# Performance work log

Measured on AMD Instinct MI355X. Metric: run time of the kernel, lower is better.

## Reference

```python
import jax, jax.numpy as jnp
import numpy as np

ROLE_BITS = 20
NHEAD = 16
D_MODEL = 1024
D_KEY = D_MODEL // NHEAD  # 64
D_FIL = 512
DFF = 4096
EPS = 1e-5


def _ln(x, g, b):
    mu = jnp.mean(x, axis=-1, keepdims=True)
    var = jnp.mean(jnp.square(x - mu), axis=-1, keepdims=True)
    return (x - mu) * jax.lax.rsqrt(var + EPS) * g + b


def setup_inputs() -> dict:
    key = jax.random.key(0)
    ks = jax.random.split(key, 10)
    N, BSZ, MEM = 16384, 16, 8
    D_IN = D_FIL + ROLE_BITS  # 532
    values = jax.random.normal(ks[0], (N, D_FIL), jnp.float32)
    role_index = jax.random.randint(ks[1], (N,), 1, 2 ** ROLE_BITS)
    # every (batch, memory_slot) pair occupied -> static shapes (compression is a no-op)
    slot = jax.random.permutation(ks[2], jnp.tile(jnp.arange(BSZ * MEM), N // (BSZ * MEM)))
    batch_index = (slot // MEM).astype(jnp.int32)
    memory_index = (slot % MEM).astype(jnp.int32)
    query_vectors = jax.random.normal(ks[3], (NHEAD, D_KEY), jnp.float32) * (1.0 / np.sqrt(D_KEY))
    s = 0.02
    Wk = jax.random.normal(ks[4], (D_MODEL, D_IN), jnp.float32) * s
    Wv = jax.random.normal(ks[5], (D_MODEL, D_IN), jnp.float32) * s
    Wo = jax.random.normal(ks[6], (D_MODEL, D_MODEL), jnp.float32) * s
    W1 = jax.random.normal(ks[7], (DFF, D_MODEL), jnp.float32) * s
    W2 = jax.random.normal(ks[8], (D_MODEL, DFF), jnp.float32) * s
    return dict(
        values=values, role_index=role_index, batch_index=batch_index,
        memory_index=memory_index, query_vectors=query_vectors,
        Wk=Wk, Wv=Wv, Wo=Wo, bo=jnp.zeros((D_MODEL,), jnp.float32),
        W1=W1, b1=jnp.zeros((DFF,), jnp.float32),
        W2=W2, b2=jnp.zeros((D_MODEL,), jnp.float32),
        g_fil=jnp.ones((D_FIL,), jnp.float32), b_fil=jnp.zeros((D_FIL,), jnp.float32),
        g_mha=jnp.ones((D_IN,), jnp.float32), b_mha=jnp.zeros((D_IN,), jnp.float32),
        g_ff=jnp.ones((D_MODEL,), jnp.float32), b_ff=jnp.zeros((D_MODEL,), jnp.float32),
        g_out=jnp.ones((D_MODEL,), jnp.float32), b_out=jnp.zeros((D_MODEL,), jnp.float32),
        bsz=BSZ, memory_slots=MEM,
    )


def _tree_positional_encodings(role_index):
    # bit-expand role indices: column j is bit j of the role index
    bits = (jnp.bitwise_and(role_index[:, None], 2 ** jnp.arange(ROLE_BITS)) != 0).astype(jnp.float32)
    # locate the highest set bit (torch: flip + argmax)
    mi = jnp.argmax(bits[:, ::-1], axis=1)
    cm = ROLE_BITS - 1 - mi  # index of highest set bit
    bits = bits * (1.0 - jax.nn.one_hot(cm, ROLE_BITS, dtype=bits.dtype))  # zero it out
    branch = jnp.arange(ROLE_BITS)[None, :] < cm[:, None]
    return jnp.where(branch, (bits - 0.5) * 2.0, bits)  # {0,1} -> {-1,1} below MSB


def reference(values, role_index, batch_index, memory_index, query_vectors,
              Wk, Wv, Wo, bo, W1, b1, W2, b2,
              g_fil, b_fil, g_mha, b_mha, g_ff, b_ff, g_out, b_out,
              bsz, memory_slots):
    N = values.shape[0]
    T = bsz * memory_slots  # num_trees (all (batch, slot) pairs occupied)

    tpd = _tree_positional_encodings(role_index)
    x = jnp.concatenate([_ln(values, g_fil, b_fil), tpd], axis=1)  # [N, d_input]
    x = _ln(x, g_mha, b_mha)
    k = (x @ Wk.T).reshape(N, NHEAD, D_KEY)
    v = (x @ Wv.T).reshape(N, NHEAD, D_KEY)
    qkm = jnp.einsum('nhd,hd->nh', k, query_vectors)  # [N, H]

    # combined batch+memory mask: node n attends to flat tree t = b*mem + m
    node_slot = batch_index * memory_slots + memory_index  # [N]
    mask = node_slot[:, None] == jnp.arange(T)[None, :]  # [N, T]
    scores = jnp.where(mask[:, :, None], qkm[:, None, :], -1e9) / np.sqrt(D_KEY)
    attn = jax.nn.softmax(scores, axis=0)  # softmax over nodes, [N, T, H]
    out = jnp.einsum('nhv,nth->thv', v, attn).reshape(T, D_MODEL)

    # post-attention: proj_o + residual with flattened queries, LN, FF, LN
    r1 = (out @ Wo.T + bo) + query_vectors.reshape(-1)
    l1 = _ln(r1, g_ff, b_ff)
    ff = jax.nn.gelu(l1 @ W1.T + b1, approximate=False) @ W2.T + b2
    l2 = _ln(ff + r1, g_out, b_out)

    rectangle_out = l2.reshape(bsz, memory_slots, D_MODEL)
    agent_pad_mask = jnp.zeros((bsz, memory_slots), dtype=bool)
    return rectangle_out, agent_pad_mask
```

## Files before the change

### kernel.cpp

```cpp
#include <hip/hip_runtime.h>
#include <hip/hip_bf16.h>

typedef __hip_bfloat16 bf16;

#define N_NODES 16384
#define D_FIL 512
#define D_IN 532
#define D_MODEL 1024
#define NHEAD 16
#define D_KEY 64
#define DFF 4096
#define NTREE 128
#define MEM_SLOTS 8
#define NODES_PER_TREE 128
#define EPS 1e-5f
#define XSE 544
#define XSU 272
#define CSTR 32
#define BSTR 40

typedef float f32x4 __attribute__((ext_vector_type(4)));
typedef short s16x8 __attribute__((ext_vector_type(8)));

union PackU { uint4 u; s16x8 s; };

__device__ inline float gelu_exact(float x) {
    return 0.5f * x * (1.0f + erff(x * 0.7071067811865476f));
}

__device__ inline void blockReduceSum2(float& a, float& b, float* sm) {
    int tid = threadIdx.x;
    int lane = tid & 63, wid = tid >> 6;
#pragma unroll
    for (int off = 32; off > 0; off >>= 1) {
        a += __shfl_down(a, off, 64);
        b += __shfl_down(b, off, 64);
    }
    if (lane == 0) { sm[wid] = a; sm[4 + wid] = b; }
    __syncthreads();
    if (tid == 0) {
        sm[8] = sm[0] + sm[1] + sm[2] + sm[3];
        sm[9] = sm[4] + sm[5] + sm[6] + sm[7];
    }
    __syncthreads();
    a = sm[8]; b = sm[9];
}

__global__ __launch_bounds__(256) void prep_kernel(
        const float* __restrict__ values, const int* __restrict__ role,
        const int* __restrict__ bidx, const int* __restrict__ midx,
        const float* __restrict__ g_fil, const float* __restrict__ b_fil,
        const float* __restrict__ g_mha, const float* __restrict__ b_mha,
        bf16* __restrict__ xs, int* __restrict__ counts,
        const float* __restrict__ q, const float* __restrict__ Wk,
        unsigned* __restrict__ wqb,
        const float* __restrict__ Wv, float* __restrict__ wvt) {
    int b = blockIdx.x;
    int tid = threadIdx.x;

    if (b < 16) {
        int h = b;
        __shared__ float qs[64];
        if (tid < 64) qs[tid] = q[h * 64 + tid];
        __syncthreads();
        for (int p = tid; p < XSU; p += 256) {
            unsigned out = 0u;
            if (p < 266) {
                float a0 = 0.f, a1 = 0.f;
                int j0 = 2 * p;
#pragma unroll 8
                for (int d = 0; d < 64; ++d) {
                    const float* wr = Wk + (size_t)(h * 64 + d) * D_IN;
                    a0 += qs[d] * wr[j0];
                    a1 += qs[d] * wr[j0 + 1];
                }
                unsigned u0 = (unsigned)__bfloat16_as_ushort(__float2bfloat16(a0));
                unsigned u1 = (unsigned)__bfloat16_as_ushort(__float2bfloat16(a1));
                out = (u1 << 16) | u0;
            }
            wqb[h * XSU + p] = out;
        }
        return;
    }

    if (b < 560) {
        __shared__ float tile[32][33];
        int vb = b - 16;
        int c0 = (vb & 31) * 32, j0 = (vb >> 5) * 32;
        int tx = tid & 31, ty = tid >> 5;
#pragma unroll
        for (int r = 0; r < 4; ++r) {
            int cc = ty + r * 8;
            int j = j0 + tx;
            tile[cc][tx] = (j < D_IN) ? Wv[(size_t)(c0 + cc) * D_IN + j] : 0.f;
        }
        __syncthreads();
#pragma unroll
        for (int r = 0; r < 4; ++r) {
            int j = j0 + ty + r * 8;
            if (j < D_IN) wvt[(size_t)j * D_MODEL + c0 + tx] = tile[tx][ty + r * 8];
        }
        return;
    }

    int wave = tid >> 6;
    int l = tid & 63;
    int n = (b - 560) * 4 + wave;

    const float4* vp = (const float4*)(values + (size_t)n * D_FIL + l * 8);
    float4 v0 = vp[0], v1 = vp[1];

    int row = 0;
    if (l == 0) {
        int slot = bidx[n] * MEM_SLOTS + midx[n];
        int pos = atomicAdd(&counts[slot * CSTR], 1);
        row = slot * NODES_PER_TREE + pos;
    }

    float s = v0.x + v0.y + v0.z + v0.w + v1.x + v1.y + v1.z + v1.w;
    float ss = v0.x * v0.x + v0.y * v0.y + v0.z * v0.z + v0.w * v0.w
             + v1.x * v1.x + v1.y * v1.y + v1.z * v1.z + v1.w * v1.w;
#pragma unroll
    for (int m = 1; m < 64; m <<= 1) {
        s += __shfl_xor(s, m, 64);
        ss += __shfl_xor(ss, m, 64);
    }
    float mu = s * (1.f / D_FIL);
    float var = ss * (1.f / D_FIL) - mu * mu;
    float rs = rsqrtf(var + EPS);

    const float4* gf = (const float4*)(g_fil + l * 8);
    const float4* bf = (const float4*)(b_fil + l * 8);
    float4 gf0 = gf[0], gf1 = gf[1], bf0 = bf[0], bf1 = bf[1];
    float y[8];
    y[0] = (v0.x - mu) * rs * gf0.x + bf0.x;
    y[1] = (v0.y - mu) * rs * gf0.y + bf0.y;
    y[2] = (v0.z - mu) * rs * gf0.z + bf0.z;
    y[3] = (v0.w - mu) * rs * gf0.w + bf0.w;
    y[4] = (v1.x - mu) * rs * gf1.x + bf1.x;
    y[5] = (v1.y - mu) * rs * gf1.y + bf1.y;
    y[6] = (v1.z - mu) * rs * gf1.z + bf1.z;
    y[7] = (v1.w - mu) * rs * gf1.w + bf1.w;

    int r = role[n];
    int cm = 31 - __clz(r);
    float s_t = 2.f * (float)(__popc(r) - 1) - (float)cm;
    float ss_t = (float)cm;

    float s2 = y[0] + y[1] + y[2] + y[3] + y[4] + y[5] + y[6] + y[7];
    float ss2 = y[0] * y[0] + y[1] * y[1] + y[2] * y[2] + y[3] * y[3]
              + y[4] * y[4] + y[5] * y[5] + y[6] * y[6] + y[7] * y[7];
#pragma unroll
    for (int m = 1; m < 64; m <<= 1) {
        s2 += __shfl_xor(s2, m, 64);
        ss2 += __shfl_xor(ss2, m, 64);
    }
    s2 += s_t; ss2 += ss_t;
    float mu2 = s2 * (1.f / D_IN);
    float var2 = ss2 * (1.f / D_IN) - mu2 * mu2;
    float rs2 = rsqrtf(var2 + EPS);

    const float4* gm = (const float4*)(g_mha + l * 8);
    const float4* bm = (const float4*)(b_mha + l * 8);
    float4 gm0 = gm[0], gm1 = gm[1], bm0 = bm[0], bm1 = bm[1];
    float x[8];
    x[0] = (y[0] - mu2) * rs2 * gm0.x + bm0.x;
    x[1] = (y[1] - mu2) * rs2 * gm0.y + bm0.y;
    x[2] = (y[2] - mu2) * rs2 * gm0.z + bm0.z;
    x[3] = (y[3] - mu2) * rs2 * gm0.w + bm0.w;
    x[4] = (y[4] - mu2) * rs2 * gm1.x + bm1.x;
    x[5] = (y[5] - mu2) * rs2 * gm1.y + bm1.y;
    x[6] = (y[6] - mu2) * rs2 * gm1.z + bm1.z;
    x[7] = (y[7] - mu2) * rs2 * gm1.w + bm1.w;

    row = __shfl(row, 0, 64);

    {
        unsigned us[8];
#pragma unroll
        for (int k = 0; k < 8; ++k)
            us[k] = (unsigned)__bfloat16_as_ushort(__float2bfloat16(x[k]));
        uint4 pk = make_uint4((us[1] << 16) | us[0], (us[3] << 16) | us[2],
                              (us[5] << 16) | us[4], (us[7] << 16) | us[6]);
        *(uint4*)((char*)xs + (size_t)row * (XSE * 2) + 16 * l) = pk;
    }

    if (l < 20) {
        int bit = (r >> l) & 1;
        float tpd = (l < cm) ? (bit ? 1.f : -1.f) : 0.f;
        float x2 = (tpd - mu2) * rs2 * g_mha[512 + l] + b_mha[512 + l];
        xs[(size_t)row * XSE + 512 + l] = __float2bfloat16(x2);
    } else if (l < 26) {
        ((unsigned*)xs)[(size_t)row * XSU + 266 + (l - 20)] = 0u;
    }
}

__global__ __launch_bounds__(256) void qkm_kernel(const unsigned* __restrict__ xsu,
                                                  const unsigned* __restrict__ wqb,
                                                  float* __restrict__ qkmp) {
    __shared__ unsigned wshw[16 * 274];
    int tid = threadIdx.x;
#pragma unroll
    for (int hh = 0; hh < 16; ++hh) {
        wshw[hh * 274 + tid] = wqb[hh * XSU + tid];
        if (tid < 16) wshw[hh * 274 + 256 + tid] = wqb[hh * XSU + 256 + tid];
    }
    __syncthreads();

    int h = tid & 15, rp = tid >> 4;
    int r0 = blockIdx.x * 32;
    const uint2* xr0 = (const uint2*)(xsu + (size_t)(r0 + 2 * rp) * XSU);
    const uint2* xr1 = (const uint2*)(xsu + (size_t)(r0 + 2 * rp + 1) * XSU);
    const uint2* wr  = (const uint2*)(wshw + h * 274);
    float a0 = 0.f, a1 = 0.f;
#pragma unroll 8
    for (int j = 0; j < 136; ++j) {
        uint2 wu = wr[j];
        uint2 xa = xr0[j];
        uint2 xb = xr1[j];
        float w0 = __uint_as_float(wu.x << 16), w1 = __uint_as_float(wu.x & 0xffff0000u);
        float w2 = __uint_as_float(wu.y << 16), w3 = __uint_as_float(wu.y & 0xffff0000u);
        a0 += __uint_as_float(xa.x << 16) * w0 + __uint_as_float(xa.x & 0xffff0000u) * w1
            + __uint_as_float(xa.y << 16) * w2 + __uint_as_float(xa.y & 0xffff0000u) * w3;
        a1 += __uint_as_float(xb.x << 16) * w0 + __uint_as_float(xb.x & 0xffff0000u) * w1
            + __uint_as_float(xb.y << 16) * w2 + __uint_as_float(xb.y & 0xffff0000u) * w3;
    }
    qkmp[(size_t)(r0 + 2 * rp) * NHEAD + h] = a0;
    qkmp[(size_t)(r0 + 2 * rp + 1) * NHEAD + h] = a1;
}

__global__ void attn_fused_kernel(const float* __restrict__ qkmp, const unsigned* __restrict__ xsu,
                                  const float* __restrict__ wvt, float* __restrict__ attn_out) {
    int hg = blockIdx.x, t = blockIdx.y, tid = threadIdx.x;
    __shared__ __align__(16) float a4[NODES_PER_TREE * 4];
    __shared__ float zs[4][536];

    for (int l = tid; l < NODES_PER_TREE * 4; l += 256) {
        int i = l >> 2, hh = l & 3;
        a4[l] = qkmp[(size_t)t * NODES_PER_TREE * NHEAD + i * 16 + hg * 4 + hh] * 0.125f;
    }
    __syncthreads();

    int hh = tid >> 6, lane = tid & 63;
    {
        float s0 = a4[lane * 4 + hh], s1 = a4[(lane + 64) * 4 + hh];
        float m = fmaxf(s0, s1);
#pragma unroll
        for (int off = 32; off > 0; off >>= 1) m = fmaxf(m, __shfl_xor(m, off, 64));
        float e0 = expf(s0 - m), e1 = expf(s1 - m);
        float sum = e0 + e1;
#pragma unroll
        for (int off = 32; off > 0; off >>= 1) sum += __shfl_xor(sum, off, 64);
        float inv = 1.0f / sum;
        a4[lane * 4 + hh] = e0 * inv;
        a4[(lane + 64) * 4 + hh] = e1 * inv;
    }
    __syncthreads();

    {
        bool hasT = tid < 10;
        float az[4][2] = {};
        float at[4][2] = {};
        const unsigned* xt = xsu + (size_t)t * NODES_PER_TREE * XSU;
        for (int i0 = 0; i0 < NODES_PER_TREE; i0 += 8) {
            unsigned u[8], u2[8];
            float4 av[8];
#pragma unroll
            for (int k = 0; k < 8; ++k) u[k] = xt[(size_t)(i0 + k) * XSU + tid];
#pragma unroll
            for (int k = 0; k < 8; ++k) u2[k] = hasT ? xt[(size_t)(i0 + k) * XSU + 256 + tid] : 0u;
#pragma unroll
            for (int k = 0; k < 8; ++k) av[k] = *(const float4*)(a4 + (i0 + k) * 4);
#pragma unroll
            for (int k = 0; k < 8; ++k) {
                float x0 = __uint_as_float(u[k] << 16);
                float x1 = __uint_as_float(u[k] & 0xffff0000u);
                float x2 = __uint_as_float(u2[k] << 16);
                float x3 = __uint_as_float(u2[k] & 0xffff0000u);
                float4 a = av[k];
                az[0][0] += a.x * x0; az[0][1] += a.x * x1;
                az[1][0] += a.y * x0; az[1][1] += a.y * x1;
                az[2][0] += a.z * x0; az[2][1] += a.z * x1;
                az[3][0] += a.w * x0; az[3][1] += a.w * x1;
                at[0][0] += a.x * x2; at[0][1] += a.x * x3;
                at[1][0] += a.y * x2; at[1][1] += a.y * x3;
                at[2][0] += a.z * x2; at[2][1] += a.z * x3;
                at[3][0] += a.w * x2; at[3][1] += a.w * x3;
            }
        }
#pragma unroll
        for (int k = 0; k < 4; ++k) {
            *(float2*)(&zs[k][2 * tid]) = make_float2(az[k][0], az[k][1]);
            if (hasT) *(float2*)(&zs[k][512 + 2 * tid]) = make_float2(at[k][0], at[k][1]);
        }
    }
    __syncthreads();

    int c = hg * 256 + tid;
    const float* wp = wvt + c;
    float acc0 = 0.f, acc1 = 0.f;
    for (int j0 = 0; j0 < 528; j0 += 8) {
        float wv[8];
#pragma unroll
        for (int k = 0; k < 8; ++k) wv[k] = wp[(size_t)(j0 + k) * D_MODEL];
#pragma unroll
        for (int k = 0; k < 8; k += 2) {
            acc0 += zs[hh][j0 + k] * wv[k];
            acc1 += zs[hh][j0 + k + 1] * wv[k + 1];
        }
    }
    {
        float wv[4];
#pragma unroll
        for (int k = 0; k < 4; ++k) wv[k] = wp[(size_t)(528 + k) * D_MODEL];
#pragma unroll
        for (int k = 0; k < 4; k += 2) {
            acc0 += zs[hh][528 + k] * wv[k];
            acc1 += zs[hh][528 + k + 1] * wv[k + 1];
        }
    }
    attn_out[(size_t)t * D_MODEL + c] = acc0 + acc1;
}

__global__ __launch_bounds__(256) void gemm_mfma_sk(const float* __restrict__ A,
                                                    const float* __restrict__ B,
                                                    float* __restrict__ Cpart,
                                                    int N, int K, int nsb) {
    __shared__ __align__(16) unsigned short bhi[64 * BSTR];
    __shared__ __align__(16) unsigned short blo[64 * BSTR];
    int tid = threadIdx.x;
    int col0 = blockIdx.x * 64;
    int k0 = blockIdx.y * nsb * 32;
    float* C = Cpart + (size_t)blockIdx.y * 128 * N;

    int w = tid >> 6, l = tid & 63;
    int l15 = l & 15, l4 = l >> 4;
    int scol = tid >> 2, sk8 = (tid & 3) * 8;

    f32x4 acc[2][4];
#pragma unroll
    for (int rt = 0; rt < 2; ++rt)
#pragma unroll
        for (int ct = 0; ct < 4; ++ct) acc[rt][ct] = (f32x4){0.f, 0.f, 0.f, 0.f};

    for (int s = 0; s < nsb; ++s) {
        int kb = k0 + s * 32;

        {
            const float* bp = B + (size_t)(col0 + scol) * K + kb + sk8;
            float4 f0 = *(const float4*)bp;
            float4 f1 = *(const float4*)(bp + 4);
            float fe[8] = {f0.x, f0.y, f0.z, f0.w, f1.x, f1.y, f1.z, f1.w};
            unsigned hu[4], lu[4];
#pragma unroll
            for (int p = 0; p < 4; ++p) {
                unsigned u0 = __float_as_uint(fe[2 * p]);
                unsigned u1 = __float_as_uint(fe[2 * p + 1]);
                unsigned h0 = u0 & 0xffff0000u, h1 = u1 & 0xffff0000u;
                float d0 = fe[2 * p] - __uint_as_float(h0);
                float d1 = fe[2 * p + 1] - __uint_as_float(h1);
                hu[p] = h1 | (u0 >> 16);
                lu[p] = (__float_as_uint(d1) & 0xffff0000u) | (__float_as_uint(d0) >> 16);
            }
            *(uint4*)(&bhi[scol * BSTR + sk8]) = make_uint4(hu[0], hu[1], hu[2], hu[3]);
            *(uint4*)(&blo[scol * BSTR + sk8]) = make_uint4(lu[0], lu[1], lu[2], lu[3]);
        }
        __syncthreads();

        s16x8 ah[2], al[2];
#pragma unroll
        for (int rt = 0; rt < 2; ++rt) {
            const float* ap = A + (size_t)(32 * w + 16 * rt + l15) * K + kb + l4 * 8;
            float4 f0 = *(const float4*)ap;
            float4 f1 = *(const float4*)(ap + 4);
            float fe[8] = {f0.x, f0.y, f0.z, f0.w, f1.x, f1.y, f1.z, f1.w};
            unsigned hu[4], lu[4];
#pragma unroll
            for (int p = 0; p < 4; ++p) {
                unsigned u0 = __float_as_uint(fe[2 * p]);
                unsigned u1 = __float_as_uint(fe[2 * p + 1]);
                unsigned h0 = u0 & 0xffff0000u, h1 = u1 & 0xffff0000u;
                float d0 = fe[2 * p] - __uint_as_float(h0);
                float d1 = fe[2 * p + 1] - __uint_as_float(h1);
                hu[p] = h1 | (u0 >> 16);
                lu[p] = (__float_as_uint(d1) & 0xffff0000u) | (__float_as_uint(d0) >> 16);
            }
            PackU uh, ul;
            uh.u = make_uint4(hu[0], hu[1], hu[2], hu[3]);
            ul.u = make_uint4(lu[0], lu[1], lu[2], lu[3]);
            ah[rt] = uh.s;
            al[rt] = ul.s;
        }

#pragma unroll
        for (int ct = 0; ct < 4; ++ct) {
            PackU rbh, rbl;
            rbh.u = *(const uint4*)(&bhi[(16 * ct + l15) * BSTR + l4 * 8]);
            rbl.u = *(const uint4*)(&blo[(16 * ct + l15) * BSTR + l4 * 8]);
#pragma unroll
            for (int rt = 0; rt < 2; ++rt) {
                acc[rt][ct] = __builtin_amdgcn_mfma_f32_16x16x32_bf16(ah[rt], rbh.s, acc[rt][ct], 0, 0, 0);
                acc[rt][ct] = __builtin_amdgcn_mfma_f32_16x16x32_bf16(al[rt], rbh.s, acc[rt][ct], 0, 0, 0);
                acc[rt][ct] = __builtin_amdgcn_mfma_f32_16x16x32_bf16(ah[rt], rbl.s, acc[rt][ct], 0, 0, 0);
            }
        }
        __syncthreads();
    }

#pragma unroll
    for (int rt = 0; rt < 2; ++rt) {
        int row = 32 * w + 16 * rt + l4 * 4;
#pragma unroll
        for (int ct = 0; ct < 4; ++ct) {
            int col = col0 + 16 * ct + l15;
#pragma unroll
            for (int r = 0; r < 4; ++r)
                C[(size_t)(row + r) * N + col] = acc[rt][ct][r];
        }
    }
}

__global__ void ln_r1_kernel(const float* __restrict__ po, const float* __restrict__ bo,
                             const float* __restrict__ qvec, const float* __restrict__ g,
                             const float* __restrict__ b, float* __restrict__ r1,
                             float* __restrict__ l1) {
    int t = blockIdx.x, tid = threadIdx.x;
    __shared__ float sm[16];
    float e[4];
#pragma unroll
    for (int c = 0; c < 4; ++c) {
        int j = c * 256 + tid;
        float v = bo[j] + qvec[j];
#pragma unroll
        for (int s = 0; s < 8; ++s)
            v += po[(size_t)s * NTREE * D_MODEL + (size_t)t * D_MODEL + j];
        e[c] = v;
        r1[(size_t)t * D_MODEL + j] = v;
    }
    float s = e[0] + e[1] + e[2] + e[3];
    float ss = e[0] * e[0] + e[1] * e[1] + e[2] * e[2] + e[3] * e[3];
    blockReduceSum2(s, ss, sm);
    float mu = s * (1.f / D_MODEL);
    float var = ss * (1.f / D_MODEL) - mu * mu;
    float rs = rsqrtf(var + EPS);
#pragma unroll
    for (int c = 0; c < 4; ++c) {
        int j = c * 256 + tid;
        l1[(size_t)t * D_MODEL + j] = (e[c] - mu) * rs * g[j] + b[j];
    }
}

__global__ void gelu_reduce_kernel(const float* __restrict__ p1, const float* __restrict__ b1,
                                   float* __restrict__ h1) {
    int idx4 = (blockIdx.x * 256 + threadIdx.x) * 4;
    int col = idx4 & (DFF - 1);
    float4 v = *(const float4*)(b1 + col);
#pragma unroll
    for (int s = 0; s < 4; ++s) {
        float4 p = *(const float4*)(p1 + (size_t)s * NTREE * DFF + idx4);
        v.x += p.x; v.y += p.y; v.z += p.z; v.w += p.w;
    }
    v.x = gelu_exact(v.x); v.y = gelu_exact(v.y);
    v.z = gelu_exact(v.z); v.w = gelu_exact(v.w);
    *(float4*)(h1 + idx4) = v;
}

__global__ void ln_out_kernel(const float* __restrict__ p2, const float* __restrict__ b2,
                              const float* __restrict__ r1, const float* __restrict__ g,
                              const float* __restrict__ b, float* __restrict__ out) {
    int t = blockIdx.x, tid = threadIdx.x;
    __shared__ float sm[16];
    float e[4];
#pragma unroll
    for (int c = 0; c < 4; ++c) {
        int j = c * 256 + tid;
        float v = b2[j] + r1[(size_t)t * D_MODEL + j];
#pragma unroll
        for (int s = 0; s < 16; ++s)
            v += p2[(size_t)s * NTREE * D_MODEL + (size_t)t * D_MODEL + j];
        e[c] = v;
    }
    float s = e[0] + e[1] + e[2] + e[3];
    float ss = e[0] * e[0] + e[1] * e[1] + e[2] * e[2] + e[3] * e[3];
    blockReduceSum2(s, ss, sm);
    float mu = s * (1.f / D_MODEL);
    float var = ss * (1.f / D_MODEL) - mu * mu;
    float rs = rsqrtf(var + EPS);
#pragma unroll
    for (int c = 0; c < 4; ++c) {
        int j = c * 256 + tid;
        out[(size_t)t * D_MODEL + j] = (e[c] - mu) * rs * g[j] + b[j];
    }
    if (t == 0 && tid < 128) out[(size_t)NTREE * D_MODEL + tid] = 0.f;
}

extern "C" void kernel_launch(void* const* d_in, const int* in_sizes, int n_in,
                              void* d_out, int out_size, void* d_ws, size_t ws_size,
                              hipStream_t stream) {
    const float* values = (const float*)d_in[0];
    const int* role     = (const int*)d_in[1];
    const int* bidx     = (const int*)d_in[2];
    const int* midx     = (const int*)d_in[3];
    const float* qvec   = (const float*)d_in[4];
    const float* Wk     = (const float*)d_in[5];
    const float* Wv     = (const float*)d_in[6];
    const float* Wo     = (const float*)d_in[7];
    const float* bo     = (const float*)d_in[8];
    const float* W1     = (const float*)d_in[9];
    const float* b1     = (const float*)d_in[10];
    const float* W2     = (const float*)d_in[11];
    const float* b2     = (const float*)d_in[12];
    const float* g_fil  = (const float*)d_in[13];
    const float* b_fil  = (const float*)d_in[14];
    const float* g_mha  = (const float*)d_in[15];
    const float* b_mha  = (const float*)d_in[16];
    const float* g_ff   = (const float*)d_in[17];
    const float* b_ff   = (const float*)d_in[18];
    const float* g_out  = (const float*)d_in[19];
    const float* b_out  = (const float*)d_in[20];

    char* w = (char*)d_ws;
    unsigned* wqb   = (unsigned*)(w + 0);
    float* qkmp     = (float*)(w + 18432);
    float* attn_out = (float*)(w + 1068032);
    float* r1       = (float*)(w + 1592320);
    float* l1       = (float*)(w + 2116608);
    float* h1       = (float*)(w + 2640896);
    int*   counts   = (int*)  (w + 2640896);
    float* wvt      = (float*)(w + 4738048);
    char*  big      = w + 6917120;
    bf16*  xs = (bf16*)big;
    float* po = (float*)big;
    float* p1 = (float*)(big + 4194304);
    float* p2 = (float*)big;

    float* out = (float*)d_out;

    hipMemsetAsync(counts, 0, 128 * CSTR * sizeof(int), stream);

    prep_kernel<<<4656, 256, 0, stream>>>(values, role, bidx, midx,
                                          g_fil, b_fil, g_mha, b_mha,
                                          xs, counts,
                                          qvec, Wk, wqb, Wv, wvt);

    qkm_kernel<<<N_NODES / 32, 256, 0, stream>>>((const unsigned*)xs, wqb, qkmp);

    attn_fused_kernel<<<dim3(4, NTREE), 256, 0, stream>>>(qkmp, (const unsigned*)xs, wvt, attn_out);

    gemm_mfma_sk<<<dim3(16, 8), 256, 0, stream>>>(attn_out, Wo, po, D_MODEL, D_MODEL, 4);

    ln_r1_kernel<<<NTREE, 256, 0, stream>>>(po, bo, qvec, g_ff, b_ff, r1, l1);

    gemm_mfma_sk<<<dim3(64, 4), 256, 0, stream>>>(l1, W1, p1, DFF, D_MODEL, 8);

    gelu_reduce_kernel<<<512, 256, 0, stream>>>(p1, b1, h1);

    gemm_mfma_sk<<<dim3(16, 16), 256, 0, stream>>>(h1, W2, p2, D_MODEL, DFF, 8);

    ln_out_kernel<<<NTREE, 256, 0, stream>>>(p2, b2, r1, g_out, b_out, out);
}
```

Measured before the change: 243.4 us.

## Fuse all stages into one persistent kernel with atomic grid barriers

After: 789.3 us. 3.24x slower.

```diff
diff --git a/kernel.cpp b/kernel.cpp
--- a/kernel.cpp
+++ b/kernel.cpp
@@ -18,6 +18,7 @@
 #define XSU 272
 #define CSTR 32
 #define BSTR 40
+#define NBLK 512
 
 typedef float f32x4 __attribute__((ext_vector_type(4)));
 typedef short s16x8 __attribute__((ext_vector_type(8)));
@@ -26,6 +27,17 @@
 
 __device__ inline float gelu_exact(float x) {
     return 0.5f * x * (1.0f + erff(x * 0.7071067811865476f));
+}
+
+__device__ inline void grid_sync(int* bar, int idx) {
+    __syncthreads();
+    if (threadIdx.x == 0) {
+        __threadfence();
+        __hip_atomic_fetch_add(&bar[idx * 32], 1, __ATOMIC_RELEASE, __HIP_MEMORY_SCOPE_AGENT);
+        while (__hip_atomic_load(&bar[idx * 32], __ATOMIC_ACQUIRE, __HIP_MEMORY_SCOPE_AGENT) < NBLK)
+            __builtin_amdgcn_s_sleep(2);
+    }
+    __syncthreads();
 }
 
 __device__ inline void blockReduceSum2(float& a, float& b, float* sm) {
@@ -46,311 +58,63 @@
     a = sm[8]; b = sm[9];
 }
 
-__global__ __launch_bounds__(256) void prep_kernel(
-        const float* __restrict__ values, const int* __restrict__ role,
-        const int* __restrict__ bidx, const int* __restrict__ midx,
-        const float* __restrict__ g_fil, const float* __restrict__ b_fil,
-        const float* __restrict__ g_mha, const float* __restrict__ b_mha,
-        bf16* __restrict__ xs, int* __restrict__ counts,
-        const float* __restrict__ q, const float* __restrict__ Wk,
-        unsigned* __restrict__ wqb,
-        const float* __restrict__ Wv, float* __restrict__ wvt) {
-    int b = blockIdx.x;
+__device__ inline void gemm_phase(const float* __restrict__ A, const float* __restrict__ B,
+                                  float* __restrict__ Cpart, int N, int K, int nsb,
+                                  int colt, int split, char* smem) {
+    unsigned short* bhi = (unsigned short*)smem;
+    unsigned short* blo = bhi + 32 * BSTR;
     int tid = threadIdx.x;
-
-    if (b < 16) {
-        int h = b;
-        __shared__ float qs[64];
-        if (tid < 64) qs[tid] = q[h * 64 + tid];
-        __syncthreads();
-        for (int p = tid; p < XSU; p += 256) {
-            unsigned out = 0u;
-            if (p < 266) {
-                float a0 = 0.f, a1 = 0.f;
-                int j0 = 2 * p;
-#pragma unroll 8
-                for (int d = 0; d < 64; ++d) {
-                    const float* wr = Wk + (size_t)(h * 64 + d) * D_IN;
-                    a0 += qs[d] * wr[j0];
-                    a1 += qs[d] * wr[j0 + 1];
-                }
-                unsigned u0 = (unsigned)__bfloat16_as_ushort(__float2bfloat16(a0));
-                unsigned u1 = (unsigned)__bfloat16_as_ushort(__float2bfloat16(a1));
-                out = (u1 << 16) | u0;
-            }
-            wqb[h * XSU + p] = out;
-        }
-        return;
-    }
-
-    if (b < 560) {
-        __shared__ float tile[32][33];
-        int vb = b - 16;
-        int c0 = (vb & 31) * 32, j0 = (vb >> 5) * 32;
-        int tx = tid & 31, ty = tid >> 5;
-#pragma unroll
-        for (int r = 0; r < 4; ++r) {
-            int cc = ty + r * 8;
-            int j = j0 + tx;
-            tile[cc][tx] = (j < D_IN) ? Wv[(size_t)(c0 + cc) * D_IN + j] : 0.f;
-        }
-        __syncthreads();
-#pragma unroll
-        for (int r = 0; r < 4; ++r) {
-            int j = j0 + ty + r * 8;
-            if (j < D_IN) wvt[(size_t)j * D_MODEL + c0 + tx] = tile[tx][ty + r * 8];
-        }
-        return;
-    }
-
-    int wave = tid >> 6;
-    int l = tid & 63;
-    int n = (b - 560) * 4 + wave;
-
-    const float4* vp = (const float4*)(values + (size_t)n * D_FIL + l * 8);
-    float4 v0 = vp[0], v1 = vp[1];
-
-    int row = 0;
-    if (l == 0) {
-        int slot = bidx[n] * MEM_SLOTS + midx[n];
-        int pos = atomicAdd(&counts[slot * CSTR], 1);
-        row = slot * NODES_PER_TREE + pos;
-    }
-
-    float s = v0.x + v0.y + v0.z + v0.w + v1.x + v1.y + v1.z + v1.w;
-    float ss = v0.x * v0.x + v0.y * v0.y + v0.z * v0.z + v0.w * v0.w
-             + v1.x * v1.x + v1.y * v1.y + v1.z * v1.z + v1.w * v1.w;
-#pragma unroll
-    for (int m = 1; m < 64; m <<= 1) {
-        s += __shfl_xor(s, m, 64);
-        ss += __shfl_xor(ss, m, 64);
-    }
-    float mu = s * (1.f / D_FIL);
-    float var = ss * (1.f / D_FIL) - mu * mu;
-    float rs = rsqrtf(var + EPS);
-
-    const float4* gf = (const float4*)(g_fil + l * 8);
-    const float4* bf = (const float4*)(b_fil + l * 8);
-    float4 gf0 = gf[0], gf1 = gf[1], bf0 = bf[0], bf1 = bf[1];
-    float y[8];
-    y[0] = (v0.x - mu) * rs * gf0.x + bf0.x;
-    y[1] = (v0.y - mu) * rs * gf0.y + bf0.y;
-    y[2] = (v0.z - mu) * rs * gf0.z + bf0.z;
-    y[3] = (v0.w - mu) * rs * gf0.w + bf0.w;
-    y[4] = (v1.x - mu) * rs * gf1.x + bf1.x;
-    y[5] = (v1.y - mu) * rs * gf1.y + bf1.y;
-    y[6] = (v1.z - mu) * rs * gf1.z + bf1.z;
-    y[7] = (v1.w - mu) * rs * gf1.w + bf1.w;
-
-    int r = role[n];
-    int cm = 31 - __clz(r);
-    float s_t = 2.f * (float)(__popc(r) - 1) - (float)cm;
-    float ss_t = (float)cm;
-
-    float s2 = y[0] + y[1] + y[2] + y[3] + y[4] + y[5] + y[6] + y[7];
-    float ss2 = y[0] * y[0] + y[1] * y[1] + y[2] * y[2] + y[3] * y[3]
-              + y[4] * y[4] + y[5] * y[5] + y[6] * y[6] + y[7] * y[7];
-#pragma unroll
-    for (int m = 1; m < 64; m <<= 1) {
-        s2 += __shfl_xor(s2, m, 64);
-        ss2 += __shfl_xor(ss2, m, 64);
-    }
-    s2 += s_t; ss2 += ss_t;
-    float mu2 = s2 * (1.f / D_IN);
-    float var2 = ss2 * (1.f / D_IN) - mu2 * mu2;
-    float rs2 = rsqrtf(var2 + EPS);
-
-    const float4* gm = (const float4*)(g_mha + l * 8);
-    const float4* bm = (const float4*)(b_mha + l * 8);
-    float4 gm0 = gm[0], gm1 = gm[1], bm0 = bm[0], bm1 = bm[1];
-    float x[8];
-    x[0] = (y[0] - mu2) * rs2 * gm0.x + bm0.x;
-    x[1] = (y[1] - mu2) * rs2 * gm0.y + bm0.y;
-    x[2] = (y[2] - mu2) * rs2 * gm0.z + bm0.z;
-    x[3] = (y[3] - mu2) * rs2 * gm0.w + bm0.w;
-    x[4] = (y[4] - mu2) * rs2 * gm1.x + bm1.x;
-    x[5] = (y[5] - mu2) * rs2 * gm1.y + bm1.y;
-    x[6] = (y[6] - mu2) * rs2 * gm1.z + bm1.z;
-    x[7] = (y[7] - mu2) * rs2 * gm1.w + bm1.w;
-
-    row = __shfl(row, 0, 64);
-
-    {
-        unsigned us[8];
-#pragma unroll
-        for (int k = 0; k < 8; ++k)
-            us[k] = (unsigned)__bfloat16_as_ushort(__float2bfloat16(x[k]));
-        uint4 pk = make_uint4((us[1] << 16) | us[0], (us[3] << 16) | us[2],
-                              (us[5] << 16) | us[4], (us[7] << 16) | us[6]);
-        *(uint4*)((char*)xs + (size_t)row * (XSE * 2) + 16 * l) = pk;
-    }
-
-    if (l < 20) {
-        int bit = (r >> l) & 1;
-        float tpd = (l < cm) ? (bit ? 1.f : -1.f) : 0.f;
-        float x2 = (tpd - mu2) * rs2 * g_mha[512 + l] + b_mha[512 + l];
-        xs[(size_t)row * XSE + 512 + l] = __float2bfloat16(x2);
-    } else if (l < 26) {
-        ((unsigned*)xs)[(size_t)row * XSU + 266 + (l - 20)] = 0u;
-    }
-}
-
-__global__ __launch_bounds__(256) void qkm_kernel(const unsigned* __restrict__ xsu,
-                                                  const unsigned* __restrict__ wqb,
-                                                  float* __restrict__ qkmp) {
-    __shared__ unsigned wshw[16 * 274];
-    int tid = threadIdx.x;
-#pragma unroll
-    for (int hh = 0; hh < 16; ++hh) {
-        wshw[hh * 274 + tid] = wqb[hh * XSU + tid];
-        if (tid < 16) wshw[hh * 274 + 256 + tid] = wqb[hh * XSU + 256 + tid];
-    }
-    __syncthreads();
-
-    int h = tid & 15, rp = tid >> 4;
-    int r0 = blockIdx.x * 32;
-    const uint2* xr0 = (const uint2*)(xsu + (size_t)(r0 + 2 * rp) * XSU);
-    const uint2* xr1 = (const uint2*)(xsu + (size_t)(r0 + 2 * rp + 1) * XSU);
-    const uint2* wr  = (const uint2*)(wshw + h * 274);
-    float a0 = 0.f, a1 = 0.f;
-#pragma unroll 8
-    for (int j = 0; j < 136; ++j) {
-        uint2 wu = wr[j];
-        uint2 xa = xr0[j];
-        uint2 xb = xr1[j];
-        float w0 = __uint_as_float(wu.x << 16), w1 = __uint_as_float(wu.x & 0xffff0000u);
-        float w2 = __uint_as_float(wu.y << 16), w3 = __uint_as_float(wu.y & 0xffff0000u);
-        a0 += __uint_as_float(xa.x << 16) * w0 + __uint_as_float(xa.x & 0xffff0000u) * w1
-            + __uint_as_float(xa.y << 16) * w2 + __uint_as_float(xa.y & 0xffff0000u) * w3;
-        a1 += __uint_as_float(xb.x << 16) * w0 + __uint_as_float(xb.x & 0xffff0000u) * w1
-            + __uint_as_float(xb.y << 16) * w2 + __uint_as_float(xb.y & 0xffff0000u) * w3;
-    }
-    qkmp[(size_t)(r0 + 2 * rp) * NHEAD + h] = a0;
-    qkmp[(size_t)(r0 + 2 * rp + 1) * NHEAD + h] = a1;
-}
-
-__global__ void attn_fused_kernel(const float* __restrict__ qkmp, const unsigned* __restrict__ xsu,
-                                  const float* __restrict__ wvt, float* __restrict__ attn_out) {
-    int hg = blockIdx.x, t = blockIdx.y, tid = threadIdx.x;
-    __shared__ __align__(16) float a4[NODES_PER_TREE * 4];
-    __shared__ float zs[4][536];
-
-    for (int l = tid; l < NODES_PER_TREE * 4; l += 256) {
-        int i = l >> 2, hh = l & 3;
-        a4[l] = qkmp[(size_t)t * NODES_PER_TREE * NHEAD + i * 16 + hg * 4 + hh] * 0.125f;
-    }
-    __syncthreads();
-
-    int hh = tid >> 6, lane = tid & 63;
-    {
-        float s0 = a4[lane * 4 + hh], s1 = a4[(lane + 64) * 4 + hh];
-        float m = fmaxf(s0, s1);
-#pragma unroll
-        for (int off = 32; off > 0; off >>= 1) m = fmaxf(m, __shfl_xor(m, off, 64));
-        float e0 = expf(s0 - m), e1 = expf(s1 - m);
-        float sum = e0 + e1;
-#pragma unroll
-        for (int off = 32; off > 0; off >>= 1) sum += __shfl_xor(sum, off, 64);
-        float inv = 1.0f / sum;
-        a4[lane * 4 + hh] = e0 * inv;
-        a4[(lane + 64) * 4 + hh] = e1 * inv;
-    }
-    __syncthreads();
-
-    {
-        bool hasT = tid < 10;
-        float az[4][2] = {};
-        float at[4][2] = {};
-        const unsigned* xt = xsu + (size_t)t * NODES_PER_TREE * XSU;
-        for (int i0 = 0; i0 < NODES_PER_TREE; i0 += 8) {
-            unsigned u[8], u2[8];
-            float4 av[8];
-#pragma unroll
-            for (int k = 0; k < 8; ++k) u[k] = xt[(size_t)(i0 + k) * XSU + tid];
-#pragma unroll
-            for (int k = 0; k < 8; ++k) u2[k] = hasT ? xt[(size_t)(i0 + k) * XSU + 256 + tid] : 0u;
-#pragma unroll
-            for (int k = 0; k < 8; ++k) av[k] = *(const float4*)(a4 + (i0 + k) * 4);
-#pragma unroll
-            for (int k = 0; k < 8; ++k) {
-                float x0 = __uint_as_float(u[k] << 16);
-                float x1 = __uint_as_float(u[k] & 0xffff0000u);
-                float x2 = __uint_as_float(u2[k] << 16);
-                float x3 = __uint_as_float(u2[k] & 0xffff0000u);
-                float4 a = av[k];
-                az[0][0] += a.x * x0; az[0][1] += a.x * x1;
-                az[1][0] += a.y * x0; az[1][1] += a.y * x1;
-                az[2][0] += a.z * x0; az[2][1] += a.z * x1;
-                az[3][0] += a.w * x0; az[3][1] += a.w * x1;
-                at[0][0] += a.x * x2; at[0][1] += a.x * x3;
-                at[1][0] += a.y * x2; at[1][1] += a.y * x3;
-                at[2][0] += a.z * x2; at[2][1] += a.z * x3;
-                at[3][0] += a.w * x2; at[3][1] += a.w * x3;
-            }
-        }
-#pragma unroll
-        for (int k = 0; k < 4; ++k) {
-            *(float2*)(&zs[k][2 * tid]) = make_float2(az[k][0], az[k][1]);
-            if (hasT) *(float2*)(&zs[k][512 + 2 * tid]) = make_float2(at[k][0], at[k][1]);
-        }
-    }
-    __syncthreads();
-
-    int c = hg * 256 + tid;
-    const float* wp = wvt + c;
-    float acc0 = 0.f, acc1 = 0.f;
-    for (int j0 = 0; j0 < 528; j0 += 8) {
-        float wv[8];
-#pragma unroll
-        for (int k = 0; k < 8; ++k) wv[k] = wp[(size_t)(j0 + k) * D_MODEL];
-#pragma unroll
-        for (int k = 0; k < 8; k += 2) {
-            acc0 += zs[hh][j0 + k] * wv[k];
-            acc1 += zs[hh][j0 + k + 1] * wv[k + 1];
-        }
-    }
-    {
-        float wv[4];
-#pragma unroll
-        for (int k = 0; k < 4; ++k) wv[k] = wp[(size_t)(528 + k) * D_MODEL];
-#pragma unroll
-        for (int k = 0; k < 4; k += 2) {
-            acc0 += zs[hh][528 + k] * wv[k];
-            acc1 += zs[hh][528 + k + 1] * wv[k + 1];
-        }
-    }
-    attn_out[(size_t)t * D_MODEL + c] = acc0 + acc1;
-}
-
-__global__ __launch_bounds__(256) void gemm_mfma_sk(const float* __restrict__ A,
-                                                    const float* __restrict__ B,
-                                                    float* __restrict__ Cpart,
-                                                    int N, int K, int nsb) {
-    __shared__ __align__(16) unsigned short bhi[64 * BSTR];
-    __shared__ __align__(16) unsigned short blo[64 * BSTR];
-    int tid = threadIdx.x;
-    int col0 = blockIdx.x * 64;
-    int k0 = blockIdx.y * nsb * 32;
-    float* C = Cpart + (size_t)blockIdx.y * 128 * N;
+    int col0 = colt * 32;
+    int k0 = split * nsb * 32;
+    float* C = Cpart + (size_t)split * 128 * N;
 
     int w = tid >> 6, l = tid & 63;
     int l15 = l & 15, l4 = l >> 4;
-    int scol = tid >> 2, sk8 = (tid & 3) * 8;
-
-    f32x4 acc[2][4];
+    int scol = tid >> 3, sk4 = (tid & 7) * 4;
+
+    f32x4 acc[2][2];
 #pragma unroll
     for (int rt = 0; rt < 2; ++rt)
 #pragma unroll
-        for (int ct = 0; ct < 4; ++ct) acc[rt][ct] = (f32x4){0.f, 0.f, 0.f, 0.f};
+        for (int ct = 0; ct < 2; ++ct) acc[rt][ct] = (f32x4){0.f, 0.f, 0.f, 0.f};
 
     for (int s = 0; s < nsb; ++s) {
         int kb = k0 + s * 32;
 
+        const float* bp = B + (size_t)(col0 + scol) * K + kb + sk4;
+        float4 fb = *(const float4*)bp;
+
+        float4 fa[2][2];
+#pragma unroll
+        for (int rt = 0; rt < 2; ++rt) {
+            const float* ap = A + (size_t)(32 * w + 16 * rt + l15) * K + kb + l4 * 8;
+            fa[rt][0] = *(const float4*)ap;
+            fa[rt][1] = *(const float4*)(ap + 4);
+        }
+
         {
-            const float* bp = B + (size_t)(col0 + scol) * K + kb + sk8;
-            float4 f0 = *(const float4*)bp;
-            float4 f1 = *(const float4*)(bp + 4);
-            float fe[8] = {f0.x, f0.y, f0.z, f0.w, f1.x, f1.y, f1.z, f1.w};
+            float fe[4] = {fb.x, fb.y, fb.z, fb.w};
+            unsigned hu[2], lu[2];
+#pragma unroll
+            for (int p = 0; p < 2; ++p) {
+                unsigned u0 = __float_as_uint(fe[2 * p]);
+                unsigned u1 = __float_as_uint(fe[2 * p + 1]);
+                unsigned h0 = u0 & 0xffff0000u, h1 = u1 & 0xffff0000u;
+                float d0 = fe[2 * p] - __uint_as_float(h0);
+                float d1 = fe[2 * p + 1] - __uint_as_float(h1);
+                hu[p] = h1 | (u0 >> 16);
+                lu[p] = (__float_as_uint(d1) & 0xffff0000u) | (__float_as_uint(d0) >> 16);
+            }
+            *(uint2*)(&bhi[scol * BSTR + sk4]) = make_uint2(hu[0], hu[1]);
+            *(uint2*)(&blo[scol * BSTR + sk4]) = make_uint2(lu[0], lu[1]);
+        }
+        __syncthreads();
+
+        s16x8 ah[2], al[2];
+#pragma unroll
+        for (int rt = 0; rt < 2; ++rt) {
+            float fe[8] = {fa[rt][0].x, fa[rt][0].y, fa[rt][0].z, fa[rt][0].w,
+                           fa[rt][1].x, fa[rt][1].y, fa[rt][1].z, fa[rt][1].w};
             unsigned hu[4], lu[4];
 #pragma unroll
             for (int p = 0; p < 4; ++p) {
@@ -362,29 +126,6 @@
                 hu[p] = h1 | (u0 >> 16);
                 lu[p] = (__float_as_uint(d1) & 0xffff0000u) | (__float_as_uint(d0) >> 16);
             }
-            *(uint4*)(&bhi[scol * BSTR + sk8]) = make_uint4(hu[0], hu[1], hu[2], hu[3]);
-            *(uint4*)(&blo[scol * BSTR + sk8]) = make_uint4(lu[0], lu[1], lu[2], lu[3]);
-        }
-        __syncthreads();
-
-        s16x8 ah[2], al[2];
-#pragma unroll
-        for (int rt = 0; rt < 2; ++rt) {
-            const float* ap = A + (size_t)(32 * w + 16 * rt + l15) * K + kb + l4 * 8;
-            float4 f0 = *(const float4*)ap;
-            float4 f1 = *(const float4*)(ap + 4);
-            float fe[8] = {f0.x, f0.y, f0.z, f0.w, f1.x, f1.y, f1.z, f1.w};
-            unsigned hu[4], lu[4];
-#pragma unroll
-            for (int p = 0; p < 4; ++p) {
-                unsigned u0 = __float_as_uint(fe[2 * p]);
-                unsigned u1 = __float_as_uint(fe[2 * p + 1]);
-                unsigned h0 = u0 & 0xffff0000u, h1 = u1 & 0xffff0000u;
-                float d0 = fe[2 * p] - __uint_as_float(h0);
-                float d1 = fe[2 * p + 1] - __uint_as_float(h1);
-                hu[p] = h1 | (u0 >> 16);
-                lu[p] = (__float_as_uint(d1) & 0xffff0000u) | (__float_as_uint(d0) >> 16);
-            }
             PackU uh, ul;
             uh.u = make_uint4(hu[0], hu[1], hu[2], hu[3]);
             ul.u = make_uint4(lu[0], lu[1], lu[2], lu[3]);
@@ -393,7 +134,7 @@
         }
 
 #pragma unroll
-        for (int ct = 0; ct < 4; ++ct) {
+        for (int ct = 0; ct < 2; ++ct) {
             PackU rbh, rbl;
             rbh.u = *(const uint4*)(&bhi[(16 * ct + l15) * BSTR + l4 * 8]);
             rbl.u = *(const uint4*)(&blo[(16 * ct + l15) * BSTR + l4 * 8]);
@@ -411,7 +152,7 @@
     for (int rt = 0; rt < 2; ++rt) {
         int row = 32 * w + 16 * rt + l4 * 4;
 #pragma unroll
-        for (int ct = 0; ct < 4; ++ct) {
+        for (int ct = 0; ct < 2; ++ct) {
             int col = col0 + 16 * ct + l15;
 #pragma unroll
             for (int r = 0; r < 4; ++r)
@@ -420,78 +161,370 @@
     }
 }
 
-__global__ void ln_r1_kernel(const float* __restrict__ po, const float* __restrict__ bo,
-                             const float* __restrict__ qvec, const float* __restrict__ g,
-                             const float* __restrict__ b, float* __restrict__ r1,
-                             float* __restrict__ l1) {
-    int t = blockIdx.x, tid = threadIdx.x;
-    __shared__ float sm[16];
-    float e[4];
-#pragma unroll
-    for (int c = 0; c < 4; ++c) {
-        int j = c * 256 + tid;
-        float v = bo[j] + qvec[j];
-#pragma unroll
-        for (int s = 0; s < 8; ++s)
-            v += po[(size_t)s * NTREE * D_MODEL + (size_t)t * D_MODEL + j];
-        e[c] = v;
-        r1[(size_t)t * D_MODEL + j] = v;
-    }
-    float s = e[0] + e[1] + e[2] + e[3];
-    float ss = e[0] * e[0] + e[1] * e[1] + e[2] * e[2] + e[3] * e[3];
-    blockReduceSum2(s, ss, sm);
-    float mu = s * (1.f / D_MODEL);
-    float var = ss * (1.f / D_MODEL) - mu * mu;
-    float rs = rsqrtf(var + EPS);
-#pragma unroll
-    for (int c = 0; c < 4; ++c) {
-        int j = c * 256 + tid;
-        l1[(size_t)t * D_MODEL + j] = (e[c] - mu) * rs * g[j] + b[j];
-    }
-}
-
-__global__ void gelu_reduce_kernel(const float* __restrict__ p1, const float* __restrict__ b1,
-                                   float* __restrict__ h1) {
-    int idx4 = (blockIdx.x * 256 + threadIdx.x) * 4;
-    int col = idx4 & (DFF - 1);
-    float4 v = *(const float4*)(b1 + col);
-#pragma unroll
-    for (int s = 0; s < 4; ++s) {
-        float4 p = *(const float4*)(p1 + (size_t)s * NTREE * DFF + idx4);
-        v.x += p.x; v.y += p.y; v.z += p.z; v.w += p.w;
-    }
-    v.x = gelu_exact(v.x); v.y = gelu_exact(v.y);
-    v.z = gelu_exact(v.z); v.w = gelu_exact(v.w);
-    *(float4*)(h1 + idx4) = v;
-}
-
-__global__ void ln_out_kernel(const float* __restrict__ p2, const float* __restrict__ b2,
-                              const float* __restrict__ r1, const float* __restrict__ g,
-                              const float* __restrict__ b, float* __restrict__ out) {
-    int t = blockIdx.x, tid = threadIdx.x;
-    __shared__ float sm[16];
-    float e[4];
-#pragma unroll
-    for (int c = 0; c < 4; ++c) {
-        int j = c * 256 + tid;
-        float v = b2[j] + r1[(size_t)t * D_MODEL + j];
-#pragma unroll
-        for (int s = 0; s < 16; ++s)
-            v += p2[(size_t)s * NTREE * D_MODEL + (size_t)t * D_MODEL + j];
-        e[c] = v;
-    }
-    float s = e[0] + e[1] + e[2] + e[3];
-    float ss = e[0] * e[0] + e[1] * e[1] + e[2] * e[2] + e[3] * e[3];
-    blockReduceSum2(s, ss, sm);
-    float mu = s * (1.f / D_MODEL);
-    float var = ss * (1.f / D_MODEL) - mu * mu;
-    float rs = rsqrtf(var + EPS);
-#pragma unroll
-    for (int c = 0; c < 4; ++c) {
-        int j = c * 256 + tid;
-        out[(size_t)t * D_MODEL + j] = (e[c] - mu) * rs * g[j] + b[j];
-    }
-    if (t == 0 && tid < 128) out[(size_t)NTREE * D_MODEL + tid] = 0.f;
+__global__ __launch_bounds__(256, 2) void mega_kernel(
+        const float* __restrict__ values, const int* __restrict__ role,
+        const int* __restrict__ bidx, const int* __restrict__ midx,
+        const float* __restrict__ qvec,
+        const float* __restrict__ Wk, const float* __restrict__ Wv,
+        const float* __restrict__ Wo, const float* __restrict__ bo,
+        const float* __restrict__ W1, const float* __restrict__ b1,
+        const float* __restrict__ W2, const float* __restrict__ b2,
+        const float* __restrict__ g_fil, const float* __restrict__ b_fil,
+        const float* __restrict__ g_mha, const float* __restrict__ b_mha,
+        const float* __restrict__ g_ff, const float* __restrict__ b_ff,
+        const float* __restrict__ g_out, const float* __restrict__ b_out,
+        int* __restrict__ bar, int* __restrict__ counts,
+        unsigned* __restrict__ wqb, float* __restrict__ qkmp,
+        float* __restrict__ attn_out, float* __restrict__ r1,
+        float* __restrict__ l1, float* __restrict__ h1,
+        float* __restrict__ wvt, bf16* __restrict__ xs,
+        float* __restrict__ po, float* __restrict__ p1, float* __restrict__ p2,
+        float* __restrict__ out) {
+    __shared__ __align__(16) char smem[17600];
+    int tid = threadIdx.x;
+
+    for (int b = blockIdx.x; b < 4656; b += NBLK) {
+        if (b < 16) {
+            int h = b;
+            float* qs = (float*)smem;
+            if (tid < 64) qs[tid] = qvec[h * 64 + tid];
+            __syncthreads();
+            for (int p = tid; p < XSU; p += 256) {
+                unsigned o = 0u;
+                if (p < 266) {
+                    float a0 = 0.f, a1 = 0.f;
+                    int j0 = 2 * p;
+#pragma unroll 8
+                    for (int d = 0; d < 64; ++d) {
+                        const float* wr = Wk + (size_t)(h * 64 + d) * D_IN;
+                        a0 += qs[d] * wr[j0];
+                        a1 += qs[d] * wr[j0 + 1];
+                    }
+                    unsigned u0 = (unsigned)__bfloat16_as_ushort(__float2bfloat16(a0));
+                    unsigned u1 = (unsigned)__bfloat16_as_ushort(__float2bfloat16(a1));
+                    o = (u1 << 16) | u0;
+                }
+                wqb[h * XSU + p] = o;
+            }
+            __syncthreads();
+        } else if (b < 560) {
+            float (*tile)[33] = (float(*)[33])smem;
+            int vb = b - 16;
+            int c0 = (vb & 31) * 32, j0 = (vb >> 5) * 32;
+            int tx = tid & 31, ty = tid >> 5;
+#pragma unroll
+            for (int r = 0; r < 4; ++r) {
+                int cc = ty + r * 8;
+                int j = j0 + tx;
+                tile[cc][tx] = (j < D_IN) ? Wv[(size_t)(c0 + cc) * D_IN + j] : 0.f;
+            }
+            __syncthreads();
+#pragma unroll
+            for (int r = 0; r < 4; ++r) {
+                int j = j0 + ty + r * 8;
+                if (j < D_IN) wvt[(size_t)j * D_MODEL + c0 + tx] = tile[tx][ty + r * 8];
+            }
+            __syncthreads();
+        } else {
+            int wave = tid >> 6;
+            int l = tid & 63;
+            int n = (b - 560) * 4 + wave;
+
+            const float4* vp = (const float4*)(values + (size_t)n * D_FIL + l * 8);
+            float4 v0 = vp[0], v1 = vp[1];
+
+            int row = 0;
+            if (l == 0) {
+                int slot = bidx[n] * MEM_SLOTS + midx[n];
+                int pos = atomicAdd(&counts[slot * CSTR], 1);
+                row = slot * NODES_PER_TREE + pos;
+            }
+
+            float s = v0.x + v0.y + v0.z + v0.w + v1.x + v1.y + v1.z + v1.w;
+            float ss = v0.x * v0.x + v0.y * v0.y + v0.z * v0.z + v0.w * v0.w
+                     + v1.x * v1.x + v1.y * v1.y + v1.z * v1.z + v1.w * v1.w;
+#pragma unroll
+            for (int m = 1; m < 64; m <<= 1) {
+                s += __shfl_xor(s, m, 64);
+                ss += __shfl_xor(ss, m, 64);
+            }
+            float mu = s * (1.f / D_FIL);
+            float var = ss * (1.f / D_FIL) - mu * mu;
+            float rs = rsqrtf(var + EPS);
+
+            const float4* gf = (const float4*)(g_fil + l * 8);
+            const float4* bf = (const float4*)(b_fil + l * 8);
+            float4 gf0 = gf[0], gf1 = gf[1], bf0 = bf[0], bf1 = bf[1];
+            float y[8];
+            y[0] = (v0.x - mu) * rs * gf0.x + bf0.x;
+            y[1] = (v0.y - mu) * rs * gf0.y + bf0.y;
+            y[2] = (v0.z - mu) * rs * gf0.z + bf0.z;
+            y[3] = (v0.w - mu) * rs * gf0.w + bf0.w;
+            y[4] = (v1.x - mu) * rs * gf1.x + bf1.x;
+            y[5] = (v1.y - mu) * rs * gf1.y + bf1.y;
+            y[6] = (v1.z - mu) * rs * gf1.z + bf1.z;
+            y[7] = (v1.w - mu) * rs * gf1.w + bf1.w;
+
+            int r = role[n];
+            int cm = 31 - __clz(r);
+            float s_t = 2.f * (float)(__popc(r) - 1) - (float)cm;
+            float ss_t = (float)cm;
+
+            float s2 = y[0] + y[1] + y[2] + y[3] + y[4] + y[5] + y[6] + y[7];
+            float ss2 = y[0] * y[0] + y[1] * y[1] + y[2] * y[2] + y[3] * y[3]
+                      + y[4] * y[4] + y[5] * y[5] + y[6] * y[6] + y[7] * y[7];
+#pragma unroll
+            for (int m = 1; m < 64; m <<= 1) {
+                s2 += __shfl_xor(s2, m, 64);
+                ss2 += __shfl_xor(ss2, m, 64);
+            }
+            s2 += s_t; ss2 += ss_t;
+            float mu2 = s2 * (1.f / D_IN);
+            float var2 = ss2 * (1.f / D_IN) - mu2 * mu2;
+            float rs2 = rsqrtf(var2 + EPS);
+
+            const float4* gm = (const float4*)(g_mha + l * 8);
+            const float4* bm = (const float4*)(b_mha + l * 8);
+            float4 gm0 = gm[0], gm1 = gm[1], bm0 = bm[0], bm1 = bm[1];
+            float x[8];
+            x[0] = (y[0] - mu2) * rs2 * gm0.x + bm0.x;
+            x[1] = (y[1] - mu2) * rs2 * gm0.y + bm0.y;
+            x[2] = (y[2] - mu2) * rs2 * gm0.z + bm0.z;
+            x[3] = (y[3] - mu2) * rs2 * gm0.w + bm0.w;
+            x[4] = (y[4] - mu2) * rs2 * gm1.x + bm1.x;
+            x[5] = (y[5] - mu2) * rs2 * gm1.y + bm1.y;
+            x[6] = (y[6] - mu2) * rs2 * gm1.z + bm1.z;
+            x[7] = (y[7] - mu2) * rs2 * gm1.w + bm1.w;
+
+            row = __shfl(row, 0, 64);
+
+            {
+                unsigned us[8];
+#pragma unroll
+                for (int k = 0; k < 8; ++k)
+                    us[k] = (unsigned)__bfloat16_as_ushort(__float2bfloat16(x[k]));
+                uint4 pk = make_uint4((us[1] << 16) | us[0], (us[3] << 16) | us[2],
+                                      (us[5] << 16) | us[4], (us[7] << 16) | us[6]);
+                *(uint4*)((char*)xs + (size_t)row * (XSE * 2) + 16 * l) = pk;
+            }
+
+            if (l < 20) {
+                int bit = (r >> l) & 1;
+                float tpd = (l < cm) ? (bit ? 1.f : -1.f) : 0.f;
+                float x2 = (tpd - mu2) * rs2 * g_mha[512 + l] + b_mha[512 + l];
+                xs[(size_t)row * XSE + 512 + l] = __float2bfloat16(x2);
+            } else if (l < 26) {
+                ((unsigned*)xs)[(size_t)row * XSU + 266 + (l - 20)] = 0u;
+            }
+        }
+    }
+    grid_sync(bar, 0);
+
+    {
+        const unsigned* xsu = (const unsigned*)xs;
+        unsigned* wshw = (unsigned*)smem;
+#pragma unroll
+        for (int hh = 0; hh < 16; ++hh) {
+            wshw[hh * 274 + tid] = wqb[hh * XSU + tid];
+            if (tid < 16) wshw[hh * 274 + 256 + tid] = wqb[hh * XSU + 256 + tid];
+        }
+        __syncthreads();
+
+        int h = tid & 15, rp = tid >> 4;
+        int r0 = blockIdx.x * 32;
+        const uint2* xr0 = (const uint2*)(xsu + (size_t)(r0 + 2 * rp) * XSU);
+        const uint2* xr1 = (const uint2*)(xsu + (size_t)(r0 + 2 * rp + 1) * XSU);
+        const uint2* wr  = (const uint2*)(wshw + h * 274);
+        float a0 = 0.f, a1 = 0.f;
+#pragma unroll 8
+        for (int j = 0; j < 136; ++j) {
+            uint2 wu = wr[j];
+            uint2 xa = xr0[j];
+            uint2 xb = xr1[j];
+            float w0 = __uint_as_float(wu.x << 16), w1 = __uint_as_float(wu.x & 0xffff0000u);
+            float w2 = __uint_as_float(wu.y << 16), w3 = __uint_as_float(wu.y & 0xffff0000u);
+            a0 += __uint_as_float(xa.x << 16) * w0 + __uint_as_float(xa.x & 0xffff0000u) * w1
+                + __uint_as_float(xa.y << 16) * w2 + __uint_as_float(xa.y & 0xffff0000u) * w3;
+            a1 += __uint_as_float(xb.x << 16) * w0 + __uint_as_float(xb.x & 0xffff0000u) * w1
+                + __uint_as_float(xb.y << 16) * w2 + __uint_as_float(xb.y & 0xffff0000u) * w3;
+        }
+        qkmp[(size_t)(r0 + 2 * rp) * NHEAD + h] = a0;
+        qkmp[(size_t)(r0 + 2 * rp + 1) * NHEAD + h] = a1;
+    }
+    grid_sync(bar, 1);
+
+    {
+        const unsigned* xsu = (const unsigned*)xs;
+        int hg = blockIdx.x & 3, t = blockIdx.x >> 2;
+        float* a4 = (float*)smem;
+        float (*zs)[536] = (float(*)[536])(smem + 2048);
+
+        for (int l = tid; l < NODES_PER_TREE * 4; l += 256) {
+            int i = l >> 2, hh = l & 3;
+            a4[l] = qkmp[(size_t)t * NODES_PER_TREE * NHEAD + i * 16 + hg * 4 + hh] * 0.125f;
+        }
+        __syncthreads();
+
+        int hh = tid >> 6, lane = tid & 63;
+        {
+            float s0 = a4[lane * 4 + hh], s1 = a4[(lane + 64) * 4 + hh];
+            float m = fmaxf(s0, s1);
+#pragma unroll
+            for (int off = 32; off > 0; off >>= 1) m = fmaxf(m, __shfl_xor(m, off, 64));
+            float e0 = expf(s0 - m), e1 = expf(s1 - m);
+            float sum = e0 + e1;
+#pragma unroll
+            for (int off = 32; off > 0; off >>= 1) sum += __shfl_xor(sum, off, 64);
+            float inv = 1.0f / sum;
+            a4[lane * 4 + hh] = e0 * inv;
+            a4[(lane + 64) * 4 + hh] = e1 * inv;
+        }
+        __syncthreads();
+
+        {
+            bool hasT = tid < 10;
+            float az[4][2] = {};
+            float at[4][2] = {};
+            const unsigned* xt = xsu + (size_t)t * NODES_PER_TREE * XSU;
+            for (int i0 = 0; i0 < NODES_PER_TREE; i0 += 8) {
+                unsigned u[8], u2[8];
+                float4 av[8];
+#pragma unroll
+                for (int k = 0; k < 8; ++k) u[k] = xt[(size_t)(i0 + k) * XSU + tid];
+#pragma unroll
+                for (int k = 0; k < 8; ++k) u2[k] = hasT ? xt[(size_t)(i0 + k) * XSU + 256 + tid] : 0u;
+#pragma unroll
+                for (int k = 0; k < 8; ++k) av[k] = *(const float4*)(a4 + (i0 + k) * 4);
+#pragma unroll
+                for (int k = 0; k < 8; ++k) {
+                    float x0 = __uint_as_float(u[k] << 16);
+                    float x1 = __uint_as_float(u[k] & 0xffff0000u);
+                    float x2 = __uint_as_float(u2[k] << 16);
+                    float x3 = __uint_as_float(u2[k] & 0xffff0000u);
+                    float4 a = av[k];
+                    az[0][0] += a.x * x0; az[0][1] += a.x * x1;
+                    az[1][0] += a.y * x0; az[1][1] += a.y * x1;
+                    az[2][0] += a.z * x0; az[2][1] += a.z * x1;
+                    az[3][0] += a.w * x0; az[3][1] += a.w * x1;
+                    at[0][0] += a.x * x2; at[0][1] += a.x * x3;
+                    at[1][0] += a.y * x2; at[1][1] += a.y * x3;
+                    at[2][0] += a.z * x2; at[2][1] += a.z * x3;
+                    at[3][0] += a.w * x2; at[3][1] += a.w * x3;
+                }
+            }
+#pragma unroll
+            for (int k = 0; k < 4; ++k) {
+                *(float2*)(&zs[k][2 * tid]) = make_float2(az[k][0], az[k][1]);
+                if (hasT) *(float2*)(&zs[k][512 + 2 * tid]) = make_float2(at[k][0], at[k][1]);
+            }
+        }
+        __syncthreads();
+
+        int c = hg * 256 + tid;
+        const float* wp = wvt + c;
+        float acc0 = 0.f, acc1 = 0.f;
+        for (int j0 = 0; j0 < 528; j0 += 8) {
+            float wv[8];
+#pragma unroll
+            for (int k = 0; k < 8; ++k) wv[k] = wp[(size_t)(j0 + k) * D_MODEL];
+#pragma unroll
+            for (int k = 0; k < 8; k += 2) {
+                acc0 += zs[hh][j0 + k] * wv[k];
+                acc1 += zs[hh][j0 + k + 1] * wv[k + 1];
+            }
+        }
+        {
+            float wv[4];
+#pragma unroll
+            for (int k = 0; k < 4; ++k) wv[k] = wp[(size_t)(528 + k) * D_MODEL];
+#pragma unroll
+            for (int k = 0; k < 4; k += 2) {
+                acc0 += zs[hh][528 + k] * wv[k];
+                acc1 += zs[hh][528 + k + 1] * wv[k + 1];
+            }
+        }
+        attn_out[(size_t)t * D_MODEL + c] = acc0 + acc1;
+    }
+    grid_sync(bar, 2);
+
+    gemm_phase(attn_out, Wo, po, D_MODEL, D_MODEL, 2, blockIdx.x & 31, blockIdx.x >> 5, smem);
+    grid_sync(bar, 3);
+
+    if (blockIdx.x < NTREE) {
+        int t = blockIdx.x;
+        float* sm = (float*)smem;
+        float e[4];
+#pragma unroll
+        for (int c = 0; c < 4; ++c) {
+            int j = c * 256 + tid;
+            float v = bo[j] + qvec[j];
+#pragma unroll
+            for (int s = 0; s < 16; ++s)
+                v += po[(size_t)s * NTREE * D_MODEL + (size_t)t * D_MODEL + j];
+            e[c] = v;
+            r1[(size_t)t * D_MODEL + j] = v;
+        }
+        float s = e[0] + e[1] + e[2] + e[3];
+        float ss = e[0] * e[0] + e[1] * e[1] + e[2] * e[2] + e[3] * e[3];
+        blockReduceSum2(s, ss, sm);
+        float mu = s * (1.f / D_MODEL);
+        float var = ss * (1.f / D_MODEL) - mu * mu;
+        float rs = rsqrtf(var + EPS);
+#pragma unroll
+        for (int c = 0; c < 4; ++c) {
+            int j = c * 256 + tid;
+            l1[(size_t)t * D_MODEL + j] = (e[c] - mu) * rs * g_ff[j] + b_ff[j];
+        }
+    }
+    grid_sync(bar, 4);
+
+    gemm_phase(l1, W1, p1, DFF, D_MODEL, 8, blockIdx.x & 127, blockIdx.x >> 7, smem);
+    grid_sync(bar, 5);
+
+    {
+        int idx4 = (blockIdx.x * 256 + tid) * 4;
+        int col = idx4 & (DFF - 1);
+        float4 v = *(const float4*)(b1 + col);
+#pragma unroll
+        for (int s = 0; s < 4; ++s) {
+            float4 p = *(const float4*)(p1 + (size_t)s * NTREE * DFF + idx4);
+            v.x += p.x; v.y += p.y; v.z += p.z; v.w += p.w;
+        }
+        v.x = gelu_exact(v.x); v.y = gelu_exact(v.y);
+        v.z = gelu_exact(v.z); v.w = gelu_exact(v.w);
+        *(float4*)(h1 + idx4) = v;
+    }
+    grid_sync(bar, 6);
+
+    gemm_phase(h1, W2, p2, D_MODEL, DFF, 8, blockIdx.x & 31, blockIdx.x >> 5, smem);
+    grid_sync(bar, 7);
+
+    if (blockIdx.x < NTREE) {
+        int t = blockIdx.x;
+        float* sm = (float*)smem;
+        float e[4];
+#pragma unroll
+        for (int c = 0; c < 4; ++c) {
+            int j = c * 256 + tid;
+            float v = b2[j] + r1[(size_t)t * D_MODEL + j];
+#pragma unroll
+            for (int s = 0; s < 16; ++s)
+                v += p2[(size_t)s * NTREE * D_MODEL + (size_t)t * D_MODEL + j];
+            e[c] = v;
+        }
+        float s = e[0] + e[1] + e[2] + e[3];
+        float ss = e[0] * e[0] + e[1] * e[1] + e[2] * e[2] + e[3] * e[3];
+        blockReduceSum2(s, ss, sm);
+        float mu = s * (1.f / D_MODEL);
+        float var = ss * (1.f / D_MODEL) - mu * mu;
+        float rs = rsqrtf(var + EPS);
+#pragma unroll
+        for (int c = 0; c < 4; ++c) {
+            int j = c * 256 + tid;
+            out[(size_t)t * D_MODEL + j] = (e[c] - mu) * rs * g_out[j] + b_out[j];
+        }
+        if (t == 0 && tid < 128) out[(size_t)NTREE * D_MODEL + tid] = 0.f;
+    }
 }
 
 extern "C" void kernel_launch(void* const* d_in, const int* in_sizes, int n_in,
@@ -520,42 +553,29 @@
     const float* b_out  = (const float*)d_in[20];
 
     char* w = (char*)d_ws;
-    unsigned* wqb   = (unsigned*)(w + 0);
-    float* qkmp     = (float*)(w + 18432);
-    float* attn_out = (float*)(w + 1068032);
-    float* r1       = (float*)(w + 1592320);
-    float* l1       = (float*)(w + 2116608);
-    float* h1       = (float*)(w + 2640896);
-    int*   counts   = (int*)  (w + 2640896);
-    float* wvt      = (float*)(w + 4738048);
-    char*  big      = w + 6917120;
+    int* bar        = (int*)(w + 0);
+    int* counts     = (int*)(w + 1024);
+    unsigned* wqb   = (unsigned*)(w + 17408);
+    float* qkmp     = (float*)(w + 34816);
+    float* attn_out = (float*)(w + 1083392);
+    float* r1       = (float*)(w + 1607680);
+    float* l1       = (float*)(w + 2131968);
+    float* h1       = (float*)(w + 2656256);
+    float* wvt      = (float*)(w + 4753408);
+    char*  big      = w + 6932480;
     bf16*  xs = (bf16*)big;
     float* po = (float*)big;
-    float* p1 = (float*)(big + 4194304);
+    float* p1 = (float*)(big + 8388608);
     float* p2 = (float*)big;
 
     float* out = (float*)d_out;
 
-    hipMemsetAsync(counts, 0, 128 * CSTR * sizeof(int), stream);
-
-    prep_kernel<<<4656, 256, 0, stream>>>(values, role, bidx, midx,
+    hipMemsetAsync(w, 0, 17408, stream);
+
+    mega_kernel<<<NBLK, 256, 0, stream>>>(values, role, bidx, midx, qvec,
+                                          Wk, Wv, Wo, bo, W1, b1, W2, b2,
                                           g_fil, b_fil, g_mha, b_mha,
-                                          xs, counts,
-                                          qvec, Wk, wqb, Wv, wvt);
-
-    qkm_kernel<<<N_NODES / 32, 256, 0, stream>>>((const unsigned*)xs, wqb, qkmp);
-
-    attn_fused_kernel<<<dim3(4, NTREE), 256, 0, stream>>>(qkmp, (const unsigned*)xs, wvt, attn_out);
-
-    gemm_mfma_sk<<<dim3(16, 8), 256, 0, stream>>>(attn_out, Wo, po, D_MODEL, D_MODEL, 4);
-
-    ln_r1_kernel<<<NTREE, 256, 0, stream>>>(po, bo, qvec, g_ff, b_ff, r1, l1);
-
-    gemm_mfma_sk<<<dim3(64, 4), 256, 0, stream>>>(l1, W1, p1, DFF, D_MODEL, 8);
-
-    gelu_reduce_kernel<<<512, 256, 0, stream>>>(p1, b1, h1);
-
-    gemm_mfma_sk<<<dim3(16, 16), 256, 0, stream>>>(h1, W2, p2, D_MODEL, DFF, 8);
-
-    ln_out_kernel<<<NTREE, 256, 0, stream>>>(p2, b2, r1, g_out, b_out, out);
+                                          g_ff, b_ff, g_out, b_out,
+                                          bar, counts, wqb, qkmp, attn_out,
+                                          r1, l1, h1, wvt, xs, po, p1, p2, out);
 }
```
